# Performance work log

Hardware: AMD Instinct MI355X
Metric: run time of the kernel (lower is better)

## Reference

```python
import jax, jax.numpy as jnp
from jax import lax
import numpy as np

B, L, IN_DIM, HID, BINS = 1, 384, 41, 64, 63
ATTN_DIM, NUM_ANCHORS = 32, 32
NUM_CONV, ATTN_EVERY = 6, 2
SIGMA, EPS = 12.0, 1e-5
DILATIONS = [1, 2, 4, 8, 16]


def select_anchors(length, k):
    # deterministic 'stride' mode of select_anchors
    k = max(1, min(k, length))
    stride = max(1, length // k)
    idx = np.arange(0, length, stride)[:k]
    if idx.size < k:
        idx = np.concatenate([idx, np.full(k - idx.size, length - 1)])
    return jnp.asarray(idx, dtype=jnp.int32)


def conv2d(x, w, b, dilation=1):
    # x: (b, Cin, H, W), w: (Cout, Cin, kh, kw) -- 'same' padding like torch padding=dilation*(k//2)
    pad = dilation * (w.shape[-1] // 2)
    y = lax.conv_general_dilated(x, w, (1, 1), [(pad, pad), (pad, pad)],
                                 rhs_dilation=(dilation, dilation),
                                 dimension_numbers=('NCHW', 'OIHW', 'NCHW'))
    return y + b[None, :, None, None]


def instance_norm(x):
    # torch InstanceNorm2d(affine=False), eps=1e-5, per (b, c) over spatial dims
    mu = x.mean(axis=(2, 3), keepdims=True)
    var = x.var(axis=(2, 3), keepdims=True)
    return (x - mu) * lax.rsqrt(var + EPS)


def anchor_attention(pair, td, tq, anchors, wq, wl, wr, wvl, wvr, wo, wg, bg,
                     tg_w1, tg_b1, tg_w2, tg_b2):
    # pair: (b, L, L, d); td: (b, L, L); tq: (b,)
    q = pair @ wq                                    # (b, L, L, a)
    p_left = pair[:, :, anchors, :]                  # (b, L, K, d)
    p_right = pair[:, anchors, :, :]                 # (b, K, L, d)
    left = p_left @ wl                               # (b, L, K, a)
    right = p_right @ wr                             # (b, K, L, a)
    scores = jnp.einsum('bija,bika->bijk', q, left)
    scores = scores + jnp.einsum('bija,bkja->bijk', q, right)
    scores = scores / jnp.sqrt(jnp.float32(ATTN_DIM))
    # template bias, 'consistency' mode
    t_left = td[:, :, anchors]                       # (b, L, K)
    t_right = jnp.swapaxes(td[:, anchors, :], 1, 2)  # (b, L, K)
    t_sum = t_left[:, :, None, :] + t_right[:, None, :, :]  # (b, L, L, K)
    bias = -jnp.abs(t_sum - td[..., None]) / SIGMA
    # TemplateGate
    coverage = (td > 0).astype(jnp.float32).mean(axis=(1, 2))        # (b,)
    length_norm = jnp.full_like(coverage, td.shape[-1] / 512.0)
    feats = jnp.stack([coverage, tq, length_norm], axis=-1)          # (b, 3)
    g = jax.nn.sigmoid(jax.nn.relu(feats @ tg_w1 + tg_b1) @ tg_w2 + tg_b2)  # (b, 1)
    scores = scores + g[:, :, None, None] * bias
    attn = jax.nn.softmax(scores, axis=-1)
    v_left = p_left @ wvl                            # (b, L, K, a)
    v_right = p_right @ wvr                          # (b, K, L, a)
    update = jnp.einsum('bijk,bika->bija', attn, v_left)
    update = update + jnp.einsum('bijk,bkja->bija', attn, v_right)
    update = update @ wo                             # (b, L, L, d)
    gate = jax.nn.sigmoid(pair @ wg + bg)
    return pair + gate * update


def setup_inputs() -> dict:
    key = jax.random.key(0)
    ks = iter(jax.random.split(key, 40))

    def rn(shape, scale=0.05):
        return jax.random.normal(next(ks), shape, dtype=jnp.float32) * scale

    return dict(
        features=jax.random.normal(next(ks), (B, L, L, IN_DIM), dtype=jnp.float32),
        template_dist=jax.random.uniform(next(ks), (B, L, L), dtype=jnp.float32) * 20.0,
        template_quality=jax.random.uniform(next(ks), (B,), dtype=jnp.float32),
        in_w=rn((HID, IN_DIM, 1, 1)), in_b=rn((HID,)),
        conv1_w=rn((NUM_CONV, HID, HID, 3, 3)), conv1_b=rn((NUM_CONV, HID)),
        conv2_w=rn((NUM_CONV, HID, HID, 3, 3)), conv2_b=rn((NUM_CONV, HID)),
        wq=rn((HID, ATTN_DIM)), wl=rn((HID, ATTN_DIM)), wr=rn((HID, ATTN_DIM)),
        wvl=rn((HID, ATTN_DIM)), wvr=rn((HID, ATTN_DIM)), wo=rn((ATTN_DIM, HID)),
        wg=rn((HID, HID)), bg=rn((HID,)),
        tg_w1=rn((3, 16)), tg_b1=rn((16,)), tg_w2=rn((16, 1)), tg_b2=rn((1,)),
        dist_w=rn((BINS, HID, 3, 3)), dist_b=rn((BINS,)),
        cf_w1=rn((32, BINS, 3, 3)), cf_b1=rn((32,)),
        cf_w2=rn((32, 32, 3, 3)), cf_b2=rn((32,)),
        cf_w3=rn((1, 32, 1, 1)), cf_b3=rn((1,)),
    )


def reference(features, template_dist, template_quality, in_w, in_b,
              conv1_w, conv1_b, conv2_w, conv2_b,
              wq, wl, wr, wvl, wvr, wo, wg, bg, tg_w1, tg_b1, tg_w2, tg_b2,
              dist_w, dist_b, cf_w1, cf_b1, cf_w2, cf_b2, cf_w3, cf_b3):
    anchors = select_anchors(L, NUM_ANCHORS)
    x = conv2d(jnp.transpose(features, (0, 3, 1, 2)), in_w, in_b)  # (b, hid, L, L)
    num_attn = max(1, NUM_CONV // max(1, ATTN_EVERY))
    attn_added = 0
    for i in range(NUM_CONV):
        d = DILATIONS[i % len(DILATIONS)]
        res = x
        out = jax.nn.elu(instance_norm(conv2d(x, conv1_w[i], conv1_b[i], d)))
        out = instance_norm(conv2d(out, conv2_w[i], conv2_b[i], 1))
        x = jax.nn.elu(out + res)
        if (i + 1) % ATTN_EVERY == 0 and attn_added < num_attn:
            pair = jnp.transpose(x, (0, 2, 3, 1))
            pair = anchor_attention(pair, template_dist, template_quality, anchors,
                                    wq, wl, wr, wvl, wvr, wo, wg, bg,
                                    tg_w1, tg_b1, tg_w2, tg_b2)
            x = jnp.transpose(pair, (0, 3, 1, 2))
            attn_added += 1
    logits = conv2d(x, dist_w, dist_b)                       # (b, bins, L, L)
    logits = 0.5 * (logits + jnp.swapaxes(logits, 2, 3))     # symmetrize_pairs
    c = jax.nn.relu(conv2d(logits, cf_w1, cf_b1))
    c = jax.nn.relu(conv2d(c, cf_w2, cf_b2))
    confidence = jax.nn.sigmoid(conv2d(c, cf_w3, cf_b3))[:, 0]   # (b, L, L)
    distance_logits = jnp.transpose(logits, (0, 2, 3, 1))        # (b, L, L, bins)
    return distance_logits, confidence
```

## Files before the change

kernel.cpp:

```cpp
#include <hip/hip_runtime.h>
#include <math.h>

#define LDIM 384
#define NPIX (LDIM*LDIM)
#define NBINS 63

typedef __attribute__((ext_vector_type(8))) __bf16 bf16x8;
typedef __attribute__((ext_vector_type(4))) float floatx4;

__device__ __forceinline__ float sigf(float x){ return 1.f/(1.f+expf(-x)); }

__global__ __launch_bounds__(256) void prep_kernel(
    const float* __restrict__ c1w, const float* __restrict__ c2w,
    const float* __restrict__ dw, const float* __restrict__ cf1w,
    const float* __restrict__ cf2w, const float* __restrict__ wg,
    const float* __restrict__ wo, const float* __restrict__ wq,
    __bf16* __restrict__ Wf){
  int idx = blockIdx.x*256 + threadIdx.x;
  if (idx >= 515072) return;
  if (idx >= 506880){
    int rel, NT, NDIM; const float* src;
    if (idx < 510976){ rel = idx - 506880; src = wg; NT=4; NDIM=64; }
    else if (idx < 513024){ rel = idx - 510976; src = wo; NT=4; NDIM=64; }
    else { rel = idx - 513024; src = wq; NT=2; NDIM=32; }
    int j = rel & 7, lane = (rel>>3) & 63;
    int r2 = rel >> 9;
    int nt = r2 % NT, kc = r2 / NT;
    int k = kc*32 + (lane>>4)*8 + j;
    int n = nt*16 + (lane&15);
    Wf[idx] = (__bf16)src[(size_t)k*NDIM + n];
    return;
  }
  const float* src; int ICreal, OCreal, ICP, NT, rel;
  if (idx < 442368){
    int layer = idx / 36864; rel = idx - layer*36864;
    int i = layer >> 1;
    src = (layer & 1) ? (c2w + (size_t)i*36864) : (c1w + (size_t)i*36864);
    ICreal=64; OCreal=64; ICP=64; NT=4;
  } else if (idx < 479232){
    rel = idx - 442368; src = dw;   ICreal=64; OCreal=63; ICP=64; NT=4;
  } else if (idx < 497664){
    rel = idx - 479232; src = cf1w; ICreal=63; OCreal=32; ICP=64; NT=2;
  } else {
    rel = idx - 497664; src = cf2w; ICreal=32; OCreal=32; ICP=32; NT=2;
  }
  int j = rel & 7, lane = (rel>>3) & 63;
  int r2 = rel >> 9;
  int nt = r2 % NT; int r3 = r2 / NT;
  int KC = ICP/32;
  int kc = r3 % KC; int tap = r3 / KC;
  int k = kc*32 + (lane>>4)*8 + j;
  int n = nt*16 + (lane&15);
  float v = 0.f;
  if (k < ICreal && n < OCreal) v = src[((size_t)n*ICreal + k)*9 + tap];
  Wf[idx] = (__bf16)v;
}

#define VMCNT(N) asm volatile("s_waitcnt vmcnt(%0)" :: "n"(N) : "memory")
#define LGKM0()  asm volatile("s_waitcnt lgkmcnt(0)" ::: "memory")
#define BARS()   { __builtin_amdgcn_s_barrier(); __builtin_amdgcn_sched_barrier(0); }

template<int ICP, int NT, int D, int WAVES>
__global__ __launch_bounds__(WAVES*64) void mfma_conv(
    const __bf16* __restrict__ Ain, const __bf16* __restrict__ Wf,
    const float* __restrict__ bias, int OC_real,
    float* __restrict__ outF, __bf16* __restrict__ outP,
    int relu, float* __restrict__ ostats){
  constexpr int KC = ICP/32;
  constexpr int OCS = NT*16;
  constexpr int REC_B = ICP*4;
  constexpr int PPX = REC_B/16;
  constexpr int HALF = PPX/2;
  constexpr int W = WAVES*16;
  constexpr int T = WAVES*64;
  constexpr int SW = W + 2*D;
  constexpr int TOT1 = SW*PPX;
  constexpr int NITER = (TOT1 + T - 1)/T;
  constexpr int BUFB = NITER*T*16;
  extern __shared__ __align__(16) char smem[];
  char* buf0 = smem;
  char* buf1 = smem + BUFB;
  const int t = threadIdx.x;
  const int wave = t>>6, lane = t&63;
  const int q = lane>>4, col16 = lane&15;
  const int y = blockIdx.y;
  const int x0 = blockIdx.x*W;

  int srcoff[NITER];
  bool oob[NITER];
  #pragma unroll
  for (int k=0;k<NITER;k++){
    int s = k*T + t;
    int px = s / PPX;
    int sub = s % PPX;
    int cg = sub ^ (px & 7);
    int gx = x0 - D + px;
    oob[k] = (px < SW) && ((unsigned)gx >= LDIM);
    int gxc = min(max(gx,0), LDIM-1);
    srcoff[k] = gxc*REC_B + cg*16;
  }

  auto STAGE = [&](char* buf, int ky){
    int yr = y + (ky-1)*D;
    int yc = min(max(yr,0), LDIM-1);
    const char* rb = (const char*)Ain + (size_t)yc*LDIM*REC_B;
    #pragma unroll
    for (int k=0;k<NITER;k++){
      char* ldsb = buf + ((size_t)k*T + wave*64)*16;
      const char* src = rb + srcoff[k];
      __builtin_amdgcn_global_load_lds(
          (const __attribute__((address_space(1))) void*)src,
          (__attribute__((address_space(3))) void*)ldsb, 16, 0, 0);
    }
  };
  auto ZOOB = [&](char* buf){
    #pragma unroll
    for (int k=0;k<NITER;k++)
      if (oob[k]){ uint4 z={0u,0u,0u,0u}; *(uint4*)(buf + ((size_t)k*T + t)*16) = z; }
  };

  floatx4 acc[NT];
  #pragma unroll
  for (int b=0;b<NT;b++){ floatx4 z = {0.f,0.f,0.f,0.f}; acc[b]=z; }

  auto MFMA_PHASE = [&](const char* buf, int ky){
    int yr = y + (ky-1)*D;
    if ((unsigned)yr >= LDIM) return;
    #pragma unroll
    for (int kx=0;kx<3;kx++){
      int cl = wave*16 + col16 + kx*D;
      int e = cl & 7;
      bf16x8 wf[KC][NT];
      #pragma unroll
      for (int kc=0;kc<KC;kc++){
        const __bf16* wkc = Wf + (size_t)((ky*3+kx)*KC + kc)*NT*512 + lane*8;
        #pragma unroll
        for (int nt=0;nt<NT;nt++)
          wf[kc][nt] = *(const bf16x8*)(wkc + (size_t)nt*512);
      }
      #pragma unroll
      for (int kc=0;kc<KC;kc++){
        int sh = (kc*4+q) ^ e;
        int sl = (HALF + kc*4+q) ^ e;
        bf16x8 ah = *(const bf16x8*)(buf + (size_t)cl*REC_B + sh*16);
        bf16x8 al = *(const bf16x8*)(buf + (size_t)cl*REC_B + sl*16);
        #pragma unroll
        for (int nt=0;nt<NT;nt++){
          acc[nt] = __builtin_amdgcn_mfma_f32_16x16x32_bf16(ah, wf[kc][nt], acc[nt], 0,0,0);
          acc[nt] = __builtin_amdgcn_mfma_f32_16x16x32_bf16(al, wf[kc][nt], acc[nt], 0,0,0);
        }
      }
    }
  };

  STAGE(buf0, 0);
  STAGE(buf1, 1);
  VMCNT(NITER);
  ZOOB(buf0); LGKM0();
  BARS();
  MFMA_PHASE(buf0, 0);
  BARS();
  STAGE(buf0, 2);
  VMCNT(NITER);
  ZOOB(buf1); LGKM0();
  BARS();
  MFMA_PHASE(buf1, 1);
  VMCNT(0);
  ZOOB(buf0); LGKM0();
  BARS();
  MFMA_PHASE(buf0, 2);

  float sAcc[NT], sqAcc[NT];
  #pragma unroll
  for (int nt=0;nt<NT;nt++){ sAcc[nt]=0.f; sqAcc[nt]=0.f; }
  #pragma unroll
  for (int nt=0; nt<NT; nt++){
    int oc = nt*16 + col16;
    float bv = (oc < OC_real) ? bias[oc] : 0.f;
    int pxb = x0 + wave*16 + q*4;
    #pragma unroll
    for (int r=0; r<4; r++){
      float vv = acc[nt][r] + bv;
      if (relu) vv = fmaxf(vv, 0.f);
      size_t pix = (size_t)y*LDIM + pxb + r;
      if (outF) outF[pix*OCS + oc] = vv;
      if (outP){
        __bf16 h = (__bf16)vv;
        __bf16* rec = outP + pix*(size_t)(OCS*2);
        rec[oc] = h; rec[OCS+oc] = (__bf16)(vv - (float)h);
      }
      sAcc[nt] += vv; sqAcc[nt] += vv*vv;
    }
  }
  if (ostats){
    float* red = (float*)smem;
    __syncthreads();
    #pragma unroll
    for (int nt=0; nt<NT; nt++){
      int oc = nt*16 + col16;
      float s = sAcc[nt], sq = sqAcc[nt];
      s  += __shfl_xor(s, 16);  s  += __shfl_xor(s, 32);
      sq += __shfl_xor(sq, 16); sq += __shfl_xor(sq, 32);
      if (q == 0){
        red[oc*WAVES + wave] = s;
        red[OCS*WAVES + oc*WAVES + wave] = sq;
      }
    }
    __syncthreads();
    float* oslot = ostats + ((blockIdx.y & 7) << 7);
    if (t < OCS){
      float s=0.f, sq=0.f;
      #pragma unroll
      for (int w=0; w<WAVES; w++){
        s  += red[t*WAVES + w];
        sq += red[OCS*WAVES + t*WAVES + w];
      }
      atomicAdd(&oslot[t], s);
      atomicAdd(&oslot[64+t], sq);
    }
  }
}

__global__ __launch_bounds__(256) void in_proj_kernel(
    const float* __restrict__ feat, const float* __restrict__ w,
    const float* __restrict__ b, __bf16* __restrict__ PX){
  __shared__ float sf[16][41];
  __shared__ float sw[64*41];
  int t = threadIdx.x;
  size_t p0 = (size_t)blockIdx.x*16;
  float wv[11];
  #pragma unroll
  for (int k=0;k<11;k++){ int idx=t+k*256; wv[k] = (idx<2624) ? w[idx] : 0.f; }
  float fv[3];
  #pragma unroll
  for (int k=0;k<3;k++){ int idx=t+k*256; fv[k] = (idx<656) ? feat[p0*41 + idx] : 0.f; }
  #pragma unroll
  for (int k=0;k<11;k++){ int idx=t+k*256; if (idx<2624) sw[idx]=wv[k]; }
  #pragma unroll
  for (int k=0;k<3;k++){
    int idx=t+k*256;
    if (idx<656){ int p = idx/41, k2 = idx - p*41; sf[p][k2]=fv[k]; }
  }
  __syncthreads();
  #pragma unroll
  for (int k=0;k<4;k++){
    int item = t + k*256;
    int c = item&63, p = item>>6;
    float acc = b[c];
    #pragma unroll
    for (int kk=0;kk<41;kk++) acc += sf[p][kk]*sw[c*41+kk];
    __bf16 h = (__bf16)acc;
    __bf16* rec = PX + (p0+p)*128;
    rec[c] = h; rec[64+c] = (__bf16)(acc - (float)h);
  }
}

__global__ __launch_bounds__(256) void norm_elu_planes(
    __bf16* __restrict__ U, const float* __restrict__ stats){
  size_t idx = (size_t)blockIdx.x*256 + threadIdx.x;
  size_t px = idx>>3; int c0 = (int)(idx&7)*8;
  __bf16* ur = U + px*128;
  uint4 uh = *(const uint4*)(ur + c0);
  uint4 ul = *(const uint4*)(ur + 64 + c0);
  __bf16* uhp=(__bf16*)&uh; __bf16* ulp=(__bf16*)&ul;
  float mu[8], rs[8];
  #pragma unroll
  for (int k=0;k<8;k++){
    int c = c0+k;
    float s=0.f, sq=0.f;
    #pragma unroll
    for (int rp=0;rp<8;rp++){ s += stats[rp*128 + c]; sq += stats[rp*128 + 64 + c]; }
    float m = s*(1.f/NPIX);
    mu[k]=m; rs[k]=rsqrtf(sq*(1.f/NPIX) - m*m + 1e-5f);
  }
  #pragma unroll
  for (int k=0;k<8;k++){
    float v = ((float)uhp[k] + (float)ulp[k] - mu[k])*rs[k];
    v = v>0.f ? v : expm1f(v);
    __bf16 h = (__bf16)v; uhp[k]=h; ulp[k]=(__bf16)(v-(float)h);
  }
  *(uint4*)(ur + c0) = uh;
  *(uint4*)(ur + 64 + c0) = ul;
}

__global__ __launch_bounds__(256) void norm_res_elu_planes(
    const __bf16* __restrict__ U, __bf16* __restrict__ PX,
    const float* __restrict__ stats){
  size_t idx = (size_t)blockIdx.x*256 + threadIdx.x;
  size_t px = idx>>3; int c0 = (int)(idx&7)*8;
  const __bf16* ur = U + px*128;
  __bf16* xr = PX + px*128;
  uint4 uh = *(const uint4*)(ur + c0);
  uint4 ul = *(const uint4*)(ur + 64 + c0);
  uint4 xh = *(uint4*)(xr + c0);
  uint4 xl = *(uint4*)(xr + 64 + c0);
  __bf16* uhp=(__bf16*)&uh; __bf16* ulp=(__bf16*)&ul;
  __bf16* xhp=(__bf16*)&xh; __bf16* xlp=(__bf16*)&xl;
  float mu[8], rs[8];
  #pragma unroll
  for (int k=0;k<8;k++){
    int c = c0+k;
    float s=0.f, sq=0.f;
    #pragma unroll
    for (int rp=0;rp<8;rp++){ s += stats[rp*128 + c]; sq += stats[rp*128 + 64 + c]; }
    float m = s*(1.f/NPIX);
    mu[k]=m; rs[k]=rsqrtf(sq*(1.f/NPIX) - m*m + 1e-5f);
  }
  #pragma unroll
  for (int k=0;k<8;k++){
    float v = ((float)uhp[k] + (float)ulp[k] - mu[k])*rs[k]
            + ((float)xhp[k] + (float)xlp[k]);
    v = v>0.f ? v : expm1f(v);
    __bf16 h = (__bf16)v; xhp[k]=h; xlp[k]=(__bf16)(v-(float)h);
  }
  *(uint4*)(xr + c0) = xh;
  *(uint4*)(xr + 64 + c0) = xl;
}

__global__ __launch_bounds__(256) void g_partial_kernel(
    const float* __restrict__ td, float* __restrict__ GC){
  size_t base = (size_t)blockIdx.x*256;
  float cnt = (td[base + threadIdx.x] > 0.f) ? 1.f : 0.f;
  __shared__ float red[256];
  red[threadIdx.x]=cnt; __syncthreads();
  for (int st=128; st; st>>=1){
    if (threadIdx.x<st) red[threadIdx.x]+=red[threadIdx.x+st];
    __syncthreads();
  }
  if (threadIdx.x==0) atomicAdd(GC, red[0]);
}

__global__ void g_final_kernel(
    const float* __restrict__ GC, const float* __restrict__ tq,
    const float* __restrict__ w1, const float* __restrict__ b1,
    const float* __restrict__ w2, const float* __restrict__ b2,
    float* __restrict__ G){
  if (threadIdx.x==0){
    float f0 = GC[0]*(1.f/NPIX), f1 = tq[0], f2 = (float)LDIM/512.f;
    float z = b2[0];
    for (int j=0;j<16;j++){
      float h = f0*w1[j] + f1*w1[16+j] + f2*w1[32+j] + b1[j];
      z += (h>0.f?h:0.f)*w2[j];
    }
    G[0] = sigf(z);
  }
}

__global__ __launch_bounds__(256) void qproj_mfma_kernel(
    const __bf16* __restrict__ PX, const __bf16* __restrict__ WqF,
    __bf16* __restrict__ Qb){
  const int t=threadIdx.x, wave=t>>6, lane=t&63, q=lane>>4, col16=lane&15;
  const size_t p0=(size_t)blockIdx.x*128;
  __shared__ __bf16 Xhi[128*72];
  __shared__ __bf16 Xlo[128*72];
  uint4 sv[8];
  #pragma unroll
  for (int k=0;k<8;k++){
    int c=t+k*256;
    sv[k] = *(const uint4*)((const char*)PX + (p0 + (c>>4))*256 + (c&15)*16);
  }
  #pragma unroll
  for (int k=0;k<8;k++){
    int c=t+k*256; int px=c>>4, sub=c&15;
    *(uint4*)(((sub<8)?Xhi:Xlo) + px*72 + (sub&7)*8) = sv[k];
  }
  __syncthreads();
  floatx4 acc[2][2];
  #pragma unroll
  for (int a=0;a<2;a++)
    #pragma unroll
    for (int b=0;b<2;b++){ floatx4 z={0.f,0.f,0.f,0.f}; acc[a][b]=z; }
  #pragma unroll
  for (int kc=0;kc<2;kc++){
    bf16x8 ah[2], al[2];
    #pragma unroll
    for (int mt=0;mt<2;mt++){
      int row = wave*32 + mt*16 + col16;
      ah[mt] = *(const bf16x8*)(Xhi + row*72 + kc*32 + q*8);
      al[mt] = *(const bf16x8*)(Xlo + row*72 + kc*32 + q*8);
    }
    #pragma unroll
    for (int nt=0;nt<2;nt++){
      bf16x8 b = *(const bf16x8*)(WqF + (kc*2+nt)*512 + lane*8);
      acc[0][nt] = __builtin_amdgcn_mfma_f32_16x16x32_bf16(ah[0], b, acc[0][nt], 0,0,0);
      acc[1][nt] = __builtin_amdgcn_mfma_f32_16x16x32_bf16(ah[1], b, acc[1][nt], 0,0,0);
      acc[0][nt] = __builtin_amdgcn_mfma_f32_16x16x32_bf16(al[0], b, acc[0][nt], 0,0,0);
      acc[1][nt] = __builtin_amdgcn_mfma_f32_16x16x32_bf16(al[1], b, acc[1][nt], 0,0,0);
    }
  }
  #pragma unroll
  for (int mt=0;mt<2;mt++){
    size_t pxb = p0 + wave*32 + mt*16 + q*4;
    #pragma unroll
    for (int nt=0;nt<2;nt++){
      int oc = nt*16 + col16;
      #pragma unroll
      for (int r=0;r<4;r++)
        Qb[(pxb+r)*32 + oc] = (__bf16)acc[mt][nt][r];
    }
  }
}

__global__ __launch_bounds__(256) void proj_left_kernel(
    const __bf16* __restrict__ PX, const float* __restrict__ wl, const float* __restrict__ wvl,
    __bf16* __restrict__ leftb, __bf16* __restrict__ vleftTb){
  int i = blockIdx.x;
  __shared__ float xa[32][65];
  __shared__ float w1s[2048], w2s[2048];
  int c = threadIdx.x & 63;
  for (int a = threadIdx.x>>6; a<32; a+=4){
    const __bf16* rec = PX + ((size_t)i*LDIM + 12*a)*128;
    xa[a][c] = (float)rec[c] + (float)rec[64+c];
  }
  for (int idx=threadIdx.x; idx<2048; idx+=256){ w1s[idx]=wl[idx]; w2s[idx]=wvl[idx]; }
  __syncthreads();
  #pragma unroll
  for (int k=0;k<4;k++){
    int idx = threadIdx.x + k*256;
    int a = idx>>5, n = idx&31;
    float a1=0.f, a2=0.f;
    #pragma unroll
    for (int cc=0;cc<64;cc++){ float v=xa[a][cc]; a1+=v*w1s[cc*32+n]; a2+=v*w2s[cc*32+n]; }
    leftb  [(size_t)i*1024 + a*32 + n] = (__bf16)a1;
    vleftTb[(size_t)i*1024 + n*32 + a] = (__bf16)a2;
  }
}

__global__ __launch_bounds__(256) void proj_right_kernel(
    const __bf16* __restrict__ PX, const float* __restrict__ wr, const float* __restrict__ wvr,
    __bf16* __restrict__ rightb, __bf16* __restrict__ vrightTb){
  int a = blockIdx.y; int row = 12*a;
  int j0 = blockIdx.x*32;
  __shared__ float xr[32][65];
  __shared__ float w1s[2048], w2s[2048];
  for (int idx=threadIdx.x; idx<2048; idx+=256){ w1s[idx]=wr[idx]; w2s[idx]=wvr[idx]; }
  int c = threadIdx.x & 63;
  for (int jl = threadIdx.x>>6; jl<32; jl+=4){
    const __bf16* rec = PX + ((size_t)row*LDIM + j0 + jl)*128;
    xr[jl][c] = (float)rec[c] + (float)rec[64+c];
  }
  __syncthreads();
  #pragma unroll
  for (int k=0;k<4;k++){
    int idx=threadIdx.x+k*256; int jl=idx>>5, n=idx&31;
    float a1=0.f, a2=0.f;
    #pragma unroll
    for (int cc=0;cc<64;cc++){ float v=xr[jl][cc]; a1+=v*w1s[cc*32+n]; a2+=v*w2s[cc*32+n]; }
    rightb  [(size_t)(j0+jl)*1024 + a*32 + n] = (__bf16)a1;
    vrightTb[(size_t)(j0+jl)*1024 + n*32 + a] = (__bf16)a2;
  }
}

__global__ __launch_bounds__(256) void attn_s1_kernel(
    const __bf16* __restrict__ Qb, const __bf16* __restrict__ leftb,
    float* __restrict__ S){
  const int t=threadIdx.x, wave=t>>6, lane=t&63, q=lane>>4, col16=lane&15;
  const int i = blockIdx.y, j0 = blockIdx.x*128;
  bf16x8 bfrag[2];
  #pragma unroll
  for (int nt=0;nt<2;nt++)
    bfrag[nt] = *(const bf16x8*)(leftb + (size_t)i*1024 + (nt*16+col16)*32 + q*8);
  bf16x8 ah[2];
  #pragma unroll
  for (int mt=0;mt<2;mt++){
    int row = j0 + wave*32 + mt*16 + col16;
    ah[mt] = *(const bf16x8*)(Qb + ((size_t)i*LDIM + row)*32 + q*8);
  }
  floatx4 acc[2][2];
  #pragma unroll
  for (int a=0;a<2;a++)
    #pragma unroll
    for (int b=0;b<2;b++){ floatx4 z={0.f,0.f,0.f,0.f}; acc[a][b]=z; }
  #pragma unroll
  for (int mt=0;mt<2;mt++)
    #pragma unroll
    for (int nt=0;nt<2;nt++)
      acc[mt][nt] = __builtin_amdgcn_mfma_f32_16x16x32_bf16(ah[mt], bfrag[nt], acc[mt][nt], 0,0,0);
  #pragma unroll
  for (int mt=0;mt<2;mt++){
    int jb = j0 + wave*32 + mt*16 + q*4;
    #pragma unroll
    for (int nt=0;nt<2;nt++){
      int a = nt*16 + col16;
      #pragma unroll
      for (int r=0;r<4;r++)
        S[((size_t)i*LDIM + jb + r)*32 + a] = acc[mt][nt][r];
    }
  }
}

__global__ __launch_bounds__(256) void attn_s2_kernel(
    const __bf16* __restrict__ Qb, const __bf16* __restrict__ rightb,
    float* __restrict__ S){
  const int t=threadIdx.x, wave=t>>6, lane=t&63, q=lane>>4, col16=lane&15;
  const int j = blockIdx.y, i0 = blockIdx.x*128;
  bf16x8 bfrag[2];
  #pragma unroll
  for (int nt=0;nt<2;nt++)
    bfrag[nt] = *(const bf16x8*)(rightb + (size_t)j*1024 + (nt*16+col16)*32 + q*8);
  bf16x8 ah[2];
  #pragma unroll
  for (int mt=0;mt<2;mt++){
    int row = i0 + wave*32 + mt*16 + col16;
    ah[mt] = *(const bf16x8*)(Qb + ((size_t)row*LDIM + j)*32 + q*8);
  }
  floatx4 acc[2][2];
  #pragma unroll
  for (int a=0;a<2;a++)
    #pragma unroll
    for (int b=0;b<2;b++){ floatx4 z={0.f,0.f,0.f,0.f}; acc[a][b]=z; }
  #pragma unroll
  for (int mt=0;mt<2;mt++)
    #pragma unroll
    for (int nt=0;nt<2;nt++)
      acc[mt][nt] = __builtin_amdgcn_mfma_f32_16x16x32_bf16(ah[mt], bfrag[nt], acc[mt][nt], 0,0,0);
  #pragma unroll
  for (int mt=0;mt<2;mt++){
    int ib = i0 + wave*32 + mt*16 + q*4;
    #pragma unroll
    for (int nt=0;nt<2;nt++){
      int a = nt*16 + col16;
      #pragma unroll
      for (int r=0;r<4;r++){
        size_t idx = ((size_t)(ib+r)*LDIM + j)*32 + a;
        S[idx] += acc[mt][nt][r];
      }
    }
  }
}

__global__ __launch_bounds__(128) void attn_soft_kernel(
    const float* __restrict__ S, const float* __restrict__ td,
    const float* __restrict__ gp, __bf16* __restrict__ attnb,
    __bf16* __restrict__ attnTb){
  int i = blockIdx.y;
  int j0 = blockIdx.x*128;
  int t = threadIdx.x;
  int j = j0 + t;
  __shared__ float tl[32];
  __shared__ float trS[32*128];
  {
    #pragma unroll
    for (int v=0; v<8; v++){
      int f = t + v*128;
      int a = f>>5, jl4 = (f&31)*4;
      *(floatx4*)(trS + a*128 + jl4) = *(const floatx4*)(td + (size_t)(12*a)*LDIM + j0 + jl4);
    }
    if (t<32) tl[t] = td[(size_t)i*LDIM + 12*t];
  }
  __syncthreads();
  float g = gp[0];
  float tdij = td[(size_t)i*LDIM+j];
  float s[32];
  const floatx4* sp4 = (const floatx4*)(S + ((size_t)i*LDIM+j)*32);
  #pragma unroll
  for (int v=0;v<8;v++){
    floatx4 sv = sp4[v];
    #pragma unroll
    for (int e=0;e<4;e++) s[v*4+e] = sv[e];
  }
  float m = -1e30f;
  #pragma unroll
  for (int a=0;a<32;a++){
    float acc = s[a]*0.17677669529663687f;
    float bias = -fabsf(tl[a] + trS[a*128 + t] - tdij) * (1.0f/12.0f);
    acc += g*bias;
    s[a]=acc;
    m = fmaxf(m, acc);
  }
  float sum=0.f;
  #pragma unroll
  for (int a=0;a<32;a++){ s[a]=expf(s[a]-m); sum+=s[a]; }
  float inv = 1.f/sum;
  bf16x8 pk[4];
  #pragma unroll
  for (int v=0;v<4;v++){
    #pragma unroll
    for (int e=0;e<8;e++) pk[v][e] = (__bf16)(s[v*8+e]*inv);
  }
  bf16x8* op = (bf16x8*)(attnb + ((size_t)i*LDIM+j)*32);
  bf16x8* opT = (bf16x8*)(attnTb + ((size_t)j*LDIM+i)*32);
  #pragma unroll
  for (int v=0;v<4;v++){ op[v]=pk[v]; opT[v]=pk[v]; }
}

__global__ __launch_bounds__(256) void attn_u1_kernel(
    const __bf16* __restrict__ attnb, const __bf16* __restrict__ vleftTb,
    float* __restrict__ UPD){
  const int t=threadIdx.x, wave=t>>6, lane=t&63, q=lane>>4, col16=lane&15;
  const int i = blockIdx.y, j0 = blockIdx.x*128;
  bf16x8 bfrag[2];
  #pragma unroll
  for (int nt=0;nt<2;nt++)
    bfrag[nt] = *(const bf16x8*)(vleftTb + (size_t)i*1024 + (nt*16+col16)*32 + q*8);
  bf16x8 ah[2];
  #pragma unroll
  for (int mt=0;mt<2;mt++){
    int row = j0 + wave*32 + mt*16 + col16;
    ah[mt] = *(const bf16x8*)(attnb + ((size_t)i*LDIM + row)*32 + q*8);
  }
  floatx4 acc[2][2];
  #pragma unroll
  for (int a=0;a<2;a++)
    #pragma unroll
    for (int b=0;b<2;b++){ floatx4 z={0.f,0.f,0.f,0.f}; acc[a][b]=z; }
  #pragma unroll
  for (int mt=0;mt<2;mt++)
    #pragma unroll
    for (int nt=0;nt<2;nt++)
      acc[mt][nt] = __builtin_amdgcn_mfma_f32_16x16x32_bf16(ah[mt], bfrag[nt], acc[mt][nt], 0,0,0);
  #pragma unroll
  for (int mt=0;mt<2;mt++){
    int jb = j0 + wave*32 + mt*16 + q*4;
    #pragma unroll
    for (int nt=0;nt<2;nt++){
      int c = nt*16 + col16;
      #pragma unroll
      for (int r=0;r<4;r++)
        UPD[((size_t)i*LDIM + jb + r)*32 + c] = acc[mt][nt][r];
    }
  }
}

__global__ __launch_bounds__(256) void attn_u2_kernel(
    const __bf16* __restrict__ attnTb, const __bf16* __restrict__ vrightTb,
    float* __restrict__ UPD){
  const int t=threadIdx.x, wave=t>>6, lane=t&63, q=lane>>4, col16=lane&15;
  const int j = blockIdx.y, i0 = blockIdx.x*128;
  bf16x8 bfrag[2];
  #pragma unroll
  for (int nt=0;nt<2;nt++)
    bfrag[nt] = *(const bf16x8*)(vrightTb + (size_t)j*1024 + (nt*16+col16)*32 + q*8);
  bf16x8 ah[2];
  #pragma unroll
  for (int mt=0;mt<2;mt++){
    int row = i0 + wave*32 + mt*16 + col16;
    ah[mt] = *(const bf16x8*)(attnTb + ((size_t)j*LDIM + row)*32 + q*8);
  }
  floatx4 acc[2][2];
  #pragma unroll
  for (int a=0;a<2;a++)
    #pragma unroll
    for (int b=0;b<2;b++){ floatx4 z={0.f,0.f,0.f,0.f}; acc[a][b]=z; }
  #pragma unroll
  for (int mt=0;mt<2;mt++)
    #pragma unroll
    for (int nt=0;nt<2;nt++)
      acc[mt][nt] = __builtin_amdgcn_mfma_f32_16x16x32_bf16(ah[mt], bfrag[nt], acc[mt][nt], 0,0,0);
  #pragma unroll
  for (int mt=0;mt<2;mt++){
    int ib = i0 + wave*32 + mt*16 + q*4;
    #pragma unroll
    for (int nt=0;nt<2;nt++){
      int c = nt*16 + col16;
      #pragma unroll
      for (int r=0;r<4;r++){
        size_t idx = ((size_t)(ib+r)*LDIM + j)*32 + c;
        UPD[idx] += acc[mt][nt][r];
      }
    }
  }
}

__global__ __launch_bounds__(256) void gate_mfma_kernel(
    __bf16* __restrict__ PX, const float* __restrict__ UPD,
    const __bf16* __restrict__ WgF, const __bf16* __restrict__ WoF,
    const float* __restrict__ bg){
  const int t=threadIdx.x, wave=t>>6, lane=t&63, q=lane>>4, col16=lane&15;
  const size_t p0=(size_t)blockIdx.x*128;
  __shared__ __bf16 Xhi[128*72];
  __shared__ __bf16 Xlo[128*72];
  __shared__ __bf16 Ub[128*40];
  uint4 sv[8];
  #pragma unroll
  for (int k=0;k<8;k++){
    int c=t+k*256;
    sv[k] = *(const uint4*)((const char*)PX + (p0 + (c>>4))*256 + (c&15)*16);
  }
  floatx4 uv[4];
  #pragma unroll
  for (int k=0;k<4;k++){
    int p = (t>>3) + k*32;
    uv[k] = *(const floatx4*)(UPD + (p0+p)*32 + (t&7)*4);
  }
  #pragma unroll
  for (int k=0;k<8;k++){
    int c=t+k*256; int px=c>>4, sub=c&15;
    *(uint4*)(((sub<8)?Xhi:Xlo) + px*72 + (sub&7)*8) = sv[k];
  }
  #pragma unroll
  for (int k=0;k<4;k++){
    int p = (t>>3) + k*32;
    __bf16* pu = Ub + p*40 + (t&7)*4;
    #pragma unroll
    for (int kk=0;kk<4;kk++) pu[kk]=(__bf16)uv[k][kk];
  }
  __syncthreads();
  floatx4 accg[2][4], accu[2][4];
  #pragma unroll
  for (int a=0;a<2;a++)
    #pragma unroll
    for (int b=0;b<4;b++){ floatx4 z={0.f,0.f,0.f,0.f}; accg[a][b]=z; accu[a][b]=z; }
  #pragma unroll
  for (int kc=0;kc<2;kc++){
    bf16x8 ah[2], al[2];
    #pragma unroll
    for (int mt=0;mt<2;mt++){
      int row = wave*32 + mt*16 + col16;
      ah[mt] = *(const bf16x8*)(Xhi + row*72 + kc*32 + q*8);
      al[mt] = *(const bf16x8*)(Xlo + row*72 + kc*32 + q*8);
    }
    #pragma unroll
    for (int nt=0;nt<4;nt++){
      bf16x8 b = *(const bf16x8*)(WgF + (kc*4+nt)*512 + lane*8);
      accg[0][nt] = __builtin_amdgcn_mfma_f32_16x16x32_bf16(ah[0], b, accg[0][nt], 0,0,0);
      accg[1][nt] = __builtin_amdgcn_mfma_f32_16x16x32_bf16(ah[1], b, accg[1][nt], 0,0,0);
      accg[0][nt] = __builtin_amdgcn_mfma_f32_16x16x32_bf16(al[0], b, accg[0][nt], 0,0,0);
      accg[1][nt] = __builtin_amdgcn_mfma_f32_16x16x32_bf16(al[1], b, accg[1][nt], 0,0,0);
    }
  }
  {
    bf16x8 au[2];
    #pragma unroll
    for (int mt=0;mt<2;mt++){
      int row = wave*32 + mt*16 + col16;
      au[mt] = *(const bf16x8*)(Ub + row*40 + q*8);
    }
    #pragma unroll
    for (int nt=0;nt<4;nt++){
      bf16x8 b = *(const bf16x8*)(WoF + nt*512 + lane*8);
      accu[0][nt] = __builtin_amdgcn_mfma_f32_16x16x32_bf16(au[0], b, accu[0][nt], 0,0,0);
      accu[1][nt] = __builtin_amdgcn_mfma_f32_16x16x32_bf16(au[1], b, accu[1][nt], 0,0,0);
    }
  }
  #pragma unroll
  for (int mt=0;mt<2;mt++){
    size_t pxb = p0 + wave*32 + mt*16 + q*4;
    #pragma unroll
    for (int nt=0;nt<4;nt++){
      int oc = nt*16 + col16;
      float bgv = bg[oc];
      #pragma unroll
      for (int r=0;r<4;r++){
        __bf16* rec = PX + (pxb+r)*128;
        float xv = (float)rec[oc] + (float)rec[64+oc];
        float g = sigf(accg[mt][nt][r] + bgv);
        float xn = xv + g*accu[mt][nt][r];
        __bf16 h = (__bf16)xn;
        rec[oc] = h; rec[64+oc] = (__bf16)(xn - (float)h);
      }
    }
  }
}

__global__ __launch_bounds__(256) void sym_kernel(
    const float* __restrict__ lg, __bf16* __restrict__ PS, float* __restrict__ dout){
  int i = blockIdx.y;
  int j = blockIdx.x*4 + (threadIdx.x>>6);
  int o = threadIdx.x & 63;
  float v = 0.5f*(lg[((size_t)i*LDIM+j)*64+o] + lg[((size_t)j*LDIM+i)*64+o]);
  size_t pix = (size_t)i*LDIM+j;
  __bf16 h = (__bf16)v;
  __bf16* rec = PS + pix*128;
  rec[o] = h; rec[64+o] = (__bf16)(v - (float)h);
  if (o<63) dout[pix*63+o] = v;
}

__global__ __launch_bounds__(256) void conf_kernel(
    const float* __restrict__ c2, const float* __restrict__ w,
    const float* __restrict__ b, float* __restrict__ out){
  int t = threadIdx.x;
  size_t pix = (size_t)blockIdx.x*8 + (t>>5);
  int c = t&31;
  float v = c2[pix*32 + c]*w[c];
  #pragma unroll
  for (int off=16; off; off>>=1) v += __shfl_xor(v, off);
  if (c==0) out[pix] = sigf(v + b[0]);
}

extern "C" void kernel_launch(void* const* d_in, const int* in_sizes, int n_in,
                              void* d_out, int out_size, void* d_ws, size_t ws_size,
                              hipStream_t stream){
  const float* feat = (const float*)d_in[0];
  const float* td   = (const float*)d_in[1];
  const float* tq   = (const float*)d_in[2];
  const float* in_w = (const float*)d_in[3];
  const float* in_b = (const float*)d_in[4];
  const float* c1w  = (const float*)d_in[5];
  const float* c1b  = (const float*)d_in[6];
  const float* c2w  = (const float*)d_in[7];
  const float* c2b  = (const float*)d_in[8];
  const float* wq   = (const float*)d_in[9];
  const float* wl   = (const float*)d_in[10];
  const float* wr   = (const float*)d_in[11];
  const float* wvl  = (const float*)d_in[12];
  const float* wvr  = (const float*)d_in[13];
  const float* wo   = (const float*)d_in[14];
  const float* wg   = (const float*)d_in[15];
  const float* bg   = (const float*)d_in[16];
  const float* tgw1 = (const float*)d_in[17];
  const float* tgb1 = (const float*)d_in[18];
  const float* tgw2 = (const float*)d_in[19];
  const float* tgb2 = (const float*)d_in[20];
  const float* dw   = (const float*)d_in[21];
  const float* db   = (const float*)d_in[22];
  const float* cf1w = (const float*)d_in[23];
  const float* cf1b = (const float*)d_in[24];
  const float* cf2w = (const float*)d_in[25];
  const float* cf2b = (const float*)d_in[26];
  const float* cf3w = (const float*)d_in[27];
  const float* cf3b = (const float*)d_in[28];

  float* ws = (float*)d_ws;
  const size_t BUF = (size_t)64*NPIX;
  float* R1 = ws;
  float* R2 = ws + BUF;
  float* R3 = ws + 2*BUF;
  float* STATS = ws + 3*BUF;
  float* G     = STATS + 12288;
  float* GC    = G + 1;
  __bf16* WF   = (__bf16*)(G + 16);
  __bf16* WGF  = WF + 506880;
  __bf16* WOF  = WF + 510976;
  __bf16* WQF  = WF + 513024;

  __bf16* PX = (__bf16*)R1;
  __bf16* PT = (__bf16*)R2;
  __bf16* PU = (__bf16*)R3;
  char* R2c = (char*)R2;
  __bf16* Qb       = (__bf16*)R2c;
  __bf16* ATTNB    = (__bf16*)(R2c +  9437184);
  __bf16* ATTNTB   = (__bf16*)(R2c + 18874368);
  __bf16* LEFTB    = (__bf16*)(R2c + 28311552);
  __bf16* RIGHTB   = (__bf16*)(R2c + 29097984);
  __bf16* VLEFTTB  = (__bf16*)(R2c + 29884416);
  __bf16* VRIGHTTB = (__bf16*)(R2c + 30670848);
  float* S   = R3;
  float* UPD = R3 + (size_t)32*NPIX;

  hipMemsetAsync(STATS, 0, (12288 + 16)*sizeof(float), stream);
  prep_kernel<<<2012, 256, 0, stream>>>(c1w, c2w, dw, cf1w, cf2w, wg, wo, wq, WF);
  g_partial_kernel<<<576, 256, 0, stream>>>(td, GC);
  g_final_kernel<<<1, 64, 0, stream>>>(GC, tq, tgw1, tgb1, tgw2, tgb2, G);

  in_proj_kernel<<<9216, 256, 0, stream>>>(feat, in_w, in_b, PX);

#define CONV_SMEM(ICP_, DD, WW) \
  (2 * (((((WW)*16+2*(DD))*((ICP_)/4)) + ((WW)*64) - 1)/((WW)*64)) * ((WW)*64) * 16)

#define CONV2_NORM(i) \
  norm_elu_planes<<<4608, 256, 0, stream>>>(PT, STATS + (2*(i))*1024); \
  mfma_conv<64,4,1,4><<<dim3(6,LDIM), 256, CONV_SMEM(64,1,4), stream>>>( \
      PT, WF + (size_t)(2*(i)+1)*36864, c2b + (i)*64, 64, \
      nullptr, PU, 0, STATS + (2*(i)+1)*1024); \
  norm_res_elu_planes<<<4608, 256, 0, stream>>>(PU, PX, STATS + (2*(i)+1)*1024);

#define CONV1(i, DD) \
  mfma_conv<64,4,DD,4><<<dim3(6,LDIM), 256, CONV_SMEM(64,DD,4), stream>>>( \
      PX, WF + (size_t)(2*(i))*36864, c1b + (i)*64, 64, \
      nullptr, PT, 0, STATS + (2*(i))*1024);

#define ATTN_BLOCK \
  qproj_mfma_kernel<<<1152, 256, 0, stream>>>(PX, WQF, Qb); \
  proj_left_kernel<<<384, 256, 0, stream>>>(PX, wl, wvl, LEFTB, VLEFTTB); \
  proj_right_kernel<<<dim3(12,32), 256, 0, stream>>>(PX, wr, wvr, RIGHTB, VRIGHTTB); \
  attn_s1_kernel<<<dim3(3,LDIM), 256, 0, stream>>>(Qb, LEFTB, S); \
  attn_s2_kernel<<<dim3(3,LDIM), 256, 0, stream>>>(Qb, RIGHTB, S); \
  attn_soft_kernel<<<dim3(3,LDIM), 128, 0, stream>>>(S, td, G, ATTNB, ATTNTB); \
  attn_u1_kernel<<<dim3(3,LDIM), 256, 0, stream>>>(ATTNB, VLEFTTB, UPD); \
  attn_u2_kernel<<<dim3(3,LDIM), 256, 0, stream>>>(ATTNTB, VRIGHTTB, UPD); \
  gate_mfma_kernel<<<1152, 256, 0, stream>>>(PX, UPD, WGF, WOF, bg);

  CONV1(0, 1)   CONV2_NORM(0)
  CONV1(1, 2)   CONV2_NORM(1)  ATTN_BLOCK
  CONV1(2, 4)   CONV2_NORM(2)
  CONV1(3, 8)   CONV2_NORM(3)  ATTN_BLOCK
  CONV1(4, 16)  CONV2_NORM(4)
  CONV1(5, 1)   CONV2_NORM(5)  ATTN_BLOCK

  mfma_conv<64,4,1,4><<<dim3(6,LDIM), 256, CONV_SMEM(64,1,4), stream>>>(
      PX, WF + 442368, db, 63, R3, nullptr, 0, nullptr);
  sym_kernel<<<dim3(96,LDIM), 256, 0, stream>>>(R3, PT, (float*)d_out);
  mfma_conv<64,2,1,4><<<dim3(6,LDIM), 256, CONV_SMEM(64,1,4), stream>>>(
      PT, WF + 479232, cf1b, 32, nullptr, PX, 1, nullptr);
  mfma_conv<32,2,1,4><<<dim3(6,LDIM), 256, CONV_SMEM(32,1,4), stream>>>(
      PX, WF + 497664, cf2b, 32, R3, nullptr, 1, nullptr);
  conf_kernel<<<18432, 256, 0, stream>>>(R3, cf3w, cf3b, (float*)d_out + (size_t)NPIX*NBINS);
}
```

Measured before the change: 1.477 ms.

## Fuse instance-norm+ELU into conv2 staging and move input projection to MFMA

The standalone norm_elu_planes pass is removed. The second conv of each residual block now applies the instance norm and ELU in shared memory to each staged input row before its MFMA phase, which saves a full read and write of the activation tensor per block. In exchange, the normalisation is recomputed for halo pixels and for every row each block stages (three times per output row), and it adds extra barriers. Separately, the scalar input projection is replaced by an MFMA kernel with split-bf16 (hi/lo) operands and weights prepacked in prep_kernel.

```diff
diff --git a/kernel.cpp b/kernel.cpp
--- a/kernel.cpp
+++ b/kernel.cpp
@@ -15,9 +15,23 @@
     const float* __restrict__ dw, const float* __restrict__ cf1w,
     const float* __restrict__ cf2w, const float* __restrict__ wg,
     const float* __restrict__ wo, const float* __restrict__ wq,
-    __bf16* __restrict__ Wf){
+    const float* __restrict__ inw, __bf16* __restrict__ Wf){
   int idx = blockIdx.x*256 + threadIdx.x;
-  if (idx >= 515072) return;
+  if (idx >= 523264) return;
+  if (idx >= 515072){
+    int rel = idx - 515072;
+    int hi = (rel < 4096) ? 1 : 0;
+    int r = rel & 4095;
+    int j = r & 7, lane = (r>>3) & 63;
+    int r2 = r >> 9;
+    int nt = r2 & 3, kc = r2 >> 2;
+    int k = kc*32 + (lane>>4)*8 + j;
+    int n = nt*16 + (lane&15);
+    float v = (k < 41) ? inw[(size_t)n*41 + k] : 0.f;
+    __bf16 h = (__bf16)v;
+    Wf[idx] = hi ? h : (__bf16)(v - (float)h);
+    return;
+  }
   if (idx >= 506880){
     int rel, NT, NDIM; const float* src;
     if (idx < 510976){ rel = idx - 506880; src = wg; NT=4; NDIM=64; }
@@ -60,12 +74,12 @@
 #define LGKM0()  asm volatile("s_waitcnt lgkmcnt(0)" ::: "memory")
 #define BARS()   { __builtin_amdgcn_s_barrier(); __builtin_amdgcn_sched_barrier(0); }
 
-template<int ICP, int NT, int D, int WAVES>
+template<int ICP, int NT, int D, int WAVES, bool NORM>
 __global__ __launch_bounds__(WAVES*64) void mfma_conv(
     const __bf16* __restrict__ Ain, const __bf16* __restrict__ Wf,
     const float* __restrict__ bias, int OC_real,
     float* __restrict__ outF, __bf16* __restrict__ outP,
-    int relu, float* __restrict__ ostats){
+    int relu, const float* __restrict__ nstats, float* __restrict__ ostats){
   constexpr int KC = ICP/32;
   constexpr int OCS = NT*16;
   constexpr int REC_B = ICP*4;
@@ -77,14 +91,28 @@
   constexpr int TOT1 = SW*PPX;
   constexpr int NITER = (TOT1 + T - 1)/T;
   constexpr int BUFB = NITER*T*16;
+  constexpr int SWH = SW*HALF;
+  constexpr int NP = (SWH + T - 1)/T;
   extern __shared__ __align__(16) char smem[];
   char* buf0 = smem;
   char* buf1 = smem + BUFB;
+  float* muS = (float*)(smem + 2*(size_t)BUFB);
   const int t = threadIdx.x;
   const int wave = t>>6, lane = t&63;
   const int q = lane>>4, col16 = lane&15;
   const int y = blockIdx.y;
   const int x0 = blockIdx.x*W;
+
+  if (NORM){
+    if (t < 64){
+      float s=0.f, sq=0.f;
+      #pragma unroll
+      for (int rp=0;rp<8;rp++){ s += nstats[rp*128 + t]; sq += nstats[rp*128 + 64 + t]; }
+      float m = s*(1.f/NPIX);
+      muS[t] = m;
+      muS[64+t] = rsqrtf(sq*(1.f/NPIX) - m*m + 1e-5f);
+    }
+  }
 
   int srcoff[NITER];
   bool oob[NITER];
@@ -117,6 +145,31 @@
     #pragma unroll
     for (int k=0;k<NITER;k++)
       if (oob[k]){ uint4 z={0u,0u,0u,0u}; *(uint4*)(buf + ((size_t)k*T + t)*16) = z; }
+  };
+  auto NORMPASS = [&](char* buf){
+    #pragma unroll
+    for (int k=0;k<NP;k++){
+      int idx = t + k*T;
+      if (idx < SWH){
+        int px = idx / HALF, g = idx % HALF;
+        int gx = x0 - D + px;
+        if ((unsigned)gx < LDIM){
+          int e = px & 7;
+          char* hp = buf + (size_t)px*REC_B + (size_t)(g ^ e)*16;
+          char* lp = hp + HALF*16;
+          bf16x8 hv = *(bf16x8*)hp, lv = *(bf16x8*)lp;
+          int c0 = g*8;
+          #pragma unroll
+          for (int j=0;j<8;j++){
+            float mu = muS[c0+j], rs = muS[64+c0+j];
+            float v = ((float)hv[j] + (float)lv[j] - mu)*rs;
+            v = v>0.f ? v : expm1f(v);
+            __bf16 h = (__bf16)v; hv[j]=h; lv[j]=(__bf16)(v-(float)h);
+          }
+          *(bf16x8*)hp = hv; *(bf16x8*)lp = lv;
+        }
+      }
+    }
   };
 
   floatx4 acc[NT];
@@ -158,16 +211,19 @@
   VMCNT(NITER);
   ZOOB(buf0); LGKM0();
   BARS();
+  if (NORM){ NORMPASS(buf0); LGKM0(); BARS(); }
   MFMA_PHASE(buf0, 0);
   BARS();
   STAGE(buf0, 2);
   VMCNT(NITER);
   ZOOB(buf1); LGKM0();
   BARS();
+  if (NORM){ NORMPASS(buf1); LGKM0(); BARS(); }
   MFMA_PHASE(buf1, 1);
   VMCNT(0);
   ZOOB(buf0); LGKM0();
   BARS();
+  if (NORM){ NORMPASS(buf0); LGKM0(); BARS(); }
   MFMA_PHASE(buf0, 2);
 
   float sAcc[NT], sqAcc[NT];
@@ -221,66 +277,63 @@
   }
 }
 
-__global__ __launch_bounds__(256) void in_proj_kernel(
-    const float* __restrict__ feat, const float* __restrict__ w,
+__global__ __launch_bounds__(256) void in_proj_mfma(
+    const float* __restrict__ feat, const __bf16* __restrict__ WinF,
     const float* __restrict__ b, __bf16* __restrict__ PX){
-  __shared__ float sf[16][41];
-  __shared__ float sw[64*41];
-  int t = threadIdx.x;
-  size_t p0 = (size_t)blockIdx.x*16;
-  float wv[11];
-  #pragma unroll
-  for (int k=0;k<11;k++){ int idx=t+k*256; wv[k] = (idx<2624) ? w[idx] : 0.f; }
-  float fv[3];
-  #pragma unroll
-  for (int k=0;k<3;k++){ int idx=t+k*256; fv[k] = (idx<656) ? feat[p0*41 + idx] : 0.f; }
-  #pragma unroll
-  for (int k=0;k<11;k++){ int idx=t+k*256; if (idx<2624) sw[idx]=wv[k]; }
-  #pragma unroll
-  for (int k=0;k<3;k++){
-    int idx=t+k*256;
-    if (idx<656){ int p = idx/41, k2 = idx - p*41; sf[p][k2]=fv[k]; }
-  }
-  __syncthreads();
-  #pragma unroll
-  for (int k=0;k<4;k++){
-    int item = t + k*256;
-    int c = item&63, p = item>>6;
-    float acc = b[c];
-    #pragma unroll
-    for (int kk=0;kk<41;kk++) acc += sf[p][kk]*sw[c*41+kk];
-    __bf16 h = (__bf16)acc;
-    __bf16* rec = PX + (p0+p)*128;
-    rec[c] = h; rec[64+c] = (__bf16)(acc - (float)h);
-  }
-}
-
-__global__ __launch_bounds__(256) void norm_elu_planes(
-    __bf16* __restrict__ U, const float* __restrict__ stats){
-  size_t idx = (size_t)blockIdx.x*256 + threadIdx.x;
-  size_t px = idx>>3; int c0 = (int)(idx&7)*8;
-  __bf16* ur = U + px*128;
-  uint4 uh = *(const uint4*)(ur + c0);
-  uint4 ul = *(const uint4*)(ur + 64 + c0);
-  __bf16* uhp=(__bf16*)&uh; __bf16* ulp=(__bf16*)&ul;
-  float mu[8], rs[8];
-  #pragma unroll
-  for (int k=0;k<8;k++){
-    int c = c0+k;
-    float s=0.f, sq=0.f;
-    #pragma unroll
-    for (int rp=0;rp<8;rp++){ s += stats[rp*128 + c]; sq += stats[rp*128 + 64 + c]; }
-    float m = s*(1.f/NPIX);
-    mu[k]=m; rs[k]=rsqrtf(sq*(1.f/NPIX) - m*m + 1e-5f);
-  }
-  #pragma unroll
-  for (int k=0;k<8;k++){
-    float v = ((float)uhp[k] + (float)ulp[k] - mu[k])*rs[k];
-    v = v>0.f ? v : expm1f(v);
-    __bf16 h = (__bf16)v; uhp[k]=h; ulp[k]=(__bf16)(v-(float)h);
-  }
-  *(uint4*)(ur + c0) = uh;
-  *(uint4*)(ur + 64 + c0) = ul;
+  const int t=threadIdx.x, wave=t>>6, lane=t&63, q=lane>>4, col16=lane&15;
+  const size_t p0=(size_t)blockIdx.x*128;
+  floatx4 acc[2][4];
+  #pragma unroll
+  for (int a=0;a<2;a++)
+    #pragma unroll
+    for (int c=0;c<4;c++){ floatx4 z={0.f,0.f,0.f,0.f}; acc[a][c]=z; }
+  #pragma unroll
+  for (int kc=0;kc<2;kc++){
+    bf16x8 ah[2], al[2];
+    #pragma unroll
+    for (int mt=0;mt<2;mt++){
+      size_t row = p0 + wave*32 + mt*16 + col16;
+      const float* fp = feat + row*41 + kc*32 + q*8;
+      float v[8];
+      #pragma unroll
+      for (int j=0;j<8;j++){
+        int k = kc*32 + q*8 + j;
+        v[j] = (k < 41) ? fp[j] : 0.f;
+      }
+      #pragma unroll
+      for (int j=0;j<8;j++){
+        __bf16 h = (__bf16)v[j];
+        ah[mt][j] = h; al[mt][j] = (__bf16)(v[j] - (float)h);
+      }
+    }
+    #pragma unroll
+    for (int nt=0;nt<4;nt++){
+      bf16x8 bh = *(const bf16x8*)(WinF + (size_t)(kc*4+nt)*512 + lane*8);
+      bf16x8 bl = *(const bf16x8*)(WinF + 4096 + (size_t)(kc*4+nt)*512 + lane*8);
+      #pragma unroll
+      for (int mt=0;mt<2;mt++){
+        acc[mt][nt] = __builtin_amdgcn_mfma_f32_16x16x32_bf16(ah[mt], bh, acc[mt][nt], 0,0,0);
+        acc[mt][nt] = __builtin_amdgcn_mfma_f32_16x16x32_bf16(al[mt], bh, acc[mt][nt], 0,0,0);
+        acc[mt][nt] = __builtin_amdgcn_mfma_f32_16x16x32_bf16(ah[mt], bl, acc[mt][nt], 0,0,0);
+      }
+    }
+  }
+  #pragma unroll
+  for (int mt=0;mt<2;mt++){
+    size_t pxb = p0 + wave*32 + mt*16 + q*4;
+    #pragma unroll
+    for (int nt=0;nt<4;nt++){
+      int oc = nt*16 + col16;
+      float bv = b[oc];
+      #pragma unroll
+      for (int r=0;r<4;r++){
+        float vv = acc[mt][nt][r] + bv;
+        __bf16* rec = PX + (pxb+r)*128;
+        __bf16 h = (__bf16)vv;
+        rec[oc] = h; rec[64+oc] = (__bf16)(vv - (float)h);
+      }
+    }
+  }
 }
 
 __global__ __launch_bounds__(256) void norm_res_elu_planes(
@@ -823,6 +876,7 @@
   __bf16* WGF  = WF + 506880;
   __bf16* WOF  = WF + 510976;
   __bf16* WQF  = WF + 513024;
+  __bf16* WINF = WF + 515072;
 
   __bf16* PX = (__bf16*)R1;
   __bf16* PT = (__bf16*)R2;
@@ -839,26 +893,25 @@
   float* UPD = R3 + (size_t)32*NPIX;
 
   hipMemsetAsync(STATS, 0, (12288 + 16)*sizeof(float), stream);
-  prep_kernel<<<2012, 256, 0, stream>>>(c1w, c2w, dw, cf1w, cf2w, wg, wo, wq, WF);
+  prep_kernel<<<2044, 256, 0, stream>>>(c1w, c2w, dw, cf1w, cf2w, wg, wo, wq, in_w, WF);
   g_partial_kernel<<<576, 256, 0, stream>>>(td, GC);
   g_final_kernel<<<1, 64, 0, stream>>>(GC, tq, tgw1, tgb1, tgw2, tgb2, G);
 
-  in_proj_kernel<<<9216, 256, 0, stream>>>(feat, in_w, in_b, PX);
+  in_proj_mfma<<<1152, 256, 0, stream>>>(feat, WINF, in_b, PX);
 
 #define CONV_SMEM(ICP_, DD, WW) \
   (2 * (((((WW)*16+2*(DD))*((ICP_)/4)) + ((WW)*64) - 1)/((WW)*64)) * ((WW)*64) * 16)
 
 #define CONV2_NORM(i) \
-  norm_elu_planes<<<4608, 256, 0, stream>>>(PT, STATS + (2*(i))*1024); \
-  mfma_conv<64,4,1,4><<<dim3(6,LDIM), 256, CONV_SMEM(64,1,4), stream>>>( \
+  mfma_conv<64,4,1,4,true><<<dim3(6,LDIM), 256, CONV_SMEM(64,1,4)+512, stream>>>( \
       PT, WF + (size_t)(2*(i)+1)*36864, c2b + (i)*64, 64, \
-      nullptr, PU, 0, STATS + (2*(i)+1)*1024); \
+      nullptr, PU, 0, STATS + (2*(i))*1024, STATS + (2*(i)+1)*1024); \
   norm_res_elu_planes<<<4608, 256, 0, stream>>>(PU, PX, STATS + (2*(i)+1)*1024);
 
 #define CONV1(i, DD) \
-  mfma_conv<64,4,DD,4><<<dim3(6,LDIM), 256, CONV_SMEM(64,DD,4), stream>>>( \
+  mfma_conv<64,4,DD,4,false><<<dim3(6,LDIM), 256, CONV_SMEM(64,DD,4), stream>>>( \
       PX, WF + (size_t)(2*(i))*36864, c1b + (i)*64, 64, \
-      nullptr, PT, 0, STATS + (2*(i))*1024);
+      nullptr, PT, 0, nullptr, STATS + (2*(i))*1024);
 
 #define ATTN_BLOCK \
   qproj_mfma_kernel<<<1152, 256, 0, stream>>>(PX, WQF, Qb); \
@@ -878,12 +931,12 @@
   CONV1(4, 16)  CONV2_NORM(4)
   CONV1(5, 1)   CONV2_NORM(5)  ATTN_BLOCK
 
-  mfma_conv<64,4,1,4><<<dim3(6,LDIM), 256, CONV_SMEM(64,1,4), stream>>>(
-      PX, WF + 442368, db, 63, R3, nullptr, 0, nullptr);
+  mfma_conv<64,4,1,4,false><<<dim3(6,LDIM), 256, CONV_SMEM(64,1,4), stream>>>(
+      PX, WF + 442368, db, 63, R3, nullptr, 0, nullptr, nullptr);
   sym_kernel<<<dim3(96,LDIM), 256, 0, stream>>>(R3, PT, (float*)d_out);
-  mfma_conv<64,2,1,4><<<dim3(6,LDIM), 256, CONV_SMEM(64,1,4), stream>>>(
-      PT, WF + 479232, cf1b, 32, nullptr, PX, 1, nullptr);
-  mfma_conv<32,2,1,4><<<dim3(6,LDIM), 256, CONV_SMEM(32,1,4), stream>>>(
-      PX, WF + 497664, cf2b, 32, R3, nullptr, 1, nullptr);
+  mfma_conv<64,2,1,4,false><<<dim3(6,LDIM), 256, CONV_SMEM(64,1,4), stream>>>(
+      PT, WF + 479232, cf1b, 32, nullptr, PX, 1, nullptr, nullptr);
+  mfma_conv<32,2,1,4,false><<<dim3(6,LDIM), 256, CONV_SMEM(32,1,4), stream>>>(
+      PX, WF + 497664, cf2b, 32, R3, nullptr, 1, nullptr, nullptr);
   conf_kernel<<<18432, 256, 0, stream>>>(R3, cf3w, cf3b, (float*)d_out + (size_t)NPIX*NBINS);
 }
```

Measured after the change: 1.461 ms. Within noise of the previous version (-1.1%).
